# Performance work log

Measured on AMD Instinct MI355X. Metric: run time of the kernel, lower is better.

## Reference

```python
import jax, jax.numpy as jnp
import numpy as np
from jax import lax

B, C = 16, 80
LEVELS = [(100, 128), (50, 64), (25, 32), (13, 16), (7, 8)]
STRIDES = [8, 16, 32, 64, 128]
SCORE_THR = 0.05
IOU_THR = 0.6
MAX_DET = 1000


def make_coords(h, w, stride):
    # FCOS: center of each cell in original-image coordinates, order (x, y)
    ys = jnp.arange(h, dtype=jnp.float32) * stride + stride // 2
    xs = jnp.arange(w, dtype=jnp.float32) * stride + stride // 2
    yy, xx = jnp.meshgrid(ys, xs, indexing='ij')
    return jnp.stack([xx.reshape(-1), yy.reshape(-1)], axis=-1)  # [h*w, 2]


def flatten_levels(feats):
    # list of [B, c, h, w] -> [B, sum(h*w), c]
    return jnp.concatenate(
        [f.transpose(0, 2, 3, 1).reshape(f.shape[0], -1, f.shape[1]) for f in feats], axis=1)


def pairwise_iou(boxes):
    # boxes [N,4]; +1 area convention, matching the torch box_nms
    x1, y1, x2, y2 = boxes[:, 0], boxes[:, 1], boxes[:, 2], boxes[:, 3]
    areas = (x2 - x1 + 1.0) * (y2 - y1 + 1.0)
    xmin = jnp.maximum(x1[:, None], x1[None, :])
    ymin = jnp.maximum(y1[:, None], y1[None, :])
    xmax = jnp.minimum(x2[:, None], x2[None, :])
    ymax = jnp.minimum(y2[:, None], y2[None, :])
    inter = jnp.clip(xmax - xmin, 0.0) * jnp.clip(ymax - ymin, 0.0)
    return inter / (areas[:, None] + areas[None, :] - inter)


def nms_keep_mask(boxes, valid, thr):
    # boxes are sorted by descending score (top_k sorted=True) -> greedy order = index order
    n = boxes.shape[0]
    iou = pairwise_iou(boxes)
    idx = jnp.arange(n)

    def body(i, sup):
        kept = jnp.logical_not(sup[i])
        return sup | (kept & (iou[i] > thr) & (idx > i))

    sup = lax.fori_loop(0, n, body, jnp.logical_not(valid))
    return valid & jnp.logical_not(sup)


def detect_forward(cls_feats, ctr_feats, reg_feats):
    cls_logits = flatten_levels(cls_feats)   # [B, P, C]
    ctr_logits = flatten_levels(ctr_feats)   # [B, P, 1]
    reg_preds = flatten_levels(reg_feats)    # [B, P, 4] (l, t, r, b)
    coords = jnp.concatenate(
        [make_coords(h, w, s) for (h, w), s in zip(LEVELS, STRIDES)], axis=0)  # [P, 2]

    cls_preds = jax.nn.sigmoid(cls_logits)
    ctr_preds = jax.nn.sigmoid(ctr_logits)[..., 0]
    cls_scores = jnp.max(cls_preds, axis=-1) * ctr_preds        # add_centerness=True
    cls_classes = jnp.argmax(cls_preds, axis=-1) + 1            # [B, P] int

    boxes = jnp.concatenate(
        [coords[None] - reg_preds[..., :2], coords[None] + reg_preds[..., 2:]], axis=-1)

    max_num = min(MAX_DET, cls_scores.shape[-1])
    scores_topk, topk_ind = lax.top_k(cls_scores, max_num)      # sorted descending
    classes_topk = jnp.take_along_axis(cls_classes, topk_ind, axis=1)
    boxes_topk = jnp.take_along_axis(boxes, topk_ind[..., None], axis=1)

    valid = scores_topk >= SCORE_THR
    # batched_nms class-offset trick
    max_coord = jnp.max(boxes_topk, axis=(1, 2), keepdims=True)
    offs = classes_topk.astype(boxes_topk.dtype)[..., None] * (max_coord + 1.0)
    boxes_for_nms = boxes_topk + offs

    keep = jax.vmap(lambda b, v: nms_keep_mask(b, v, IOU_THR))(boxes_for_nms, valid)
    keep_f = keep.astype(scores_topk.dtype)
    # fixed-shape masked outputs (torch version returns ragged per-batch lists)
    return scores_topk * keep_f, classes_topk * keep, boxes_topk * keep_f[..., None]


def setup_inputs() -> dict:
    key = jax.random.key(0)
    ks = jax.random.split(key, 3 * len(LEVELS))
    inp = {}
    for i, (h, w) in enumerate(LEVELS):
        inp[f'cls{i}'] = jax.random.normal(ks[3 * i], (B, C, h, w), jnp.float32)
        inp[f'ctr{i}'] = jax.random.normal(ks[3 * i + 1], (B, 1, h, w), jnp.float32)
        # positive ltrb offsets of plausible magnitude
        inp[f'reg{i}'] = jax.random.uniform(ks[3 * i + 2], (B, 4, h, w), jnp.float32) * 64.0 + 1.0
    return inp


def reference(cls0, cls1, cls2, cls3, cls4, ctr0, ctr1, ctr2, ctr3, ctr4,
              reg0, reg1, reg2, reg3, reg4):
    return detect_forward([cls0, cls1, cls2, cls3, cls4],
                          [ctr0, ctr1, ctr2, ctr3, ctr4],
                          [reg0, reg1, reg2, reg3, reg4])
```

## Files before the change

### kernel.cpp

```cpp
#include <hip/hip_runtime.h>
#include <stdint.h>

#define NANCH 17064
#define BATCH 16
#define NCLS 80
#define KDET 1000
#define SCORE_THR 0.05f
#define IOU_THR 0.6f

typedef unsigned long long u64;
typedef unsigned int u32;

__device__ __forceinline__ float sigf(float x) { return 1.0f / (1.0f + expf(-x)); }

__device__ __forceinline__ void decode_anchor(int n, int& l, int& h, int& w) {
  if (n < 12800)      { l = 0; h = n >> 7;               w = n & 127; }
  else if (n < 16000) { l = 1; int r = n - 12800; h = r >> 6; w = r & 63; }
  else if (n < 16800) { l = 2; int r = n - 16000; h = r >> 5; w = r & 31; }
  else if (n < 17008) { l = 3; int r = n - 16800; h = r >> 4; w = r & 15; }
  else                { l = 4; int r = n - 17008; h = r >> 3; w = r & 7; }
}

__device__ __forceinline__ u32 fenc(float f) {
  u32 u = __float_as_uint(f);
  return (u & 0x80000000u) ? ~u : (u | 0x80000000u);
}
__device__ __forceinline__ float fdec(u32 e) {
  u32 u = (e & 0x80000000u) ? (e ^ 0x80000000u) : ~e;
  return __uint_as_float(u);
}

__global__ __launch_bounds__(256, 4) void k_score(
    const float* __restrict__ cls0, const float* __restrict__ ctr0,
    const float* __restrict__ cls1, const float* __restrict__ ctr1,
    const float* __restrict__ cls2, const float* __restrict__ ctr2,
    const float* __restrict__ cls3, const float* __restrict__ ctr3,
    const float* __restrict__ cls4, const float* __restrict__ ctr4,
    u32* __restrict__ sb, u32* __restrict__ cl8)
{
  __shared__ float sm[4][64][5];
  __shared__ u32 sa[4][64];

  const int x = threadIdx.x;
  const int y = threadIdx.y;
  const int b = blockIdx.y;
  int q = blockIdx.x * 64 + x;
  const bool act = (q < NANCH / 4);
  int qc = act ? q : (NANCH / 4 - 1);
  int n = qc * 4;

  const float* cp; const float* tp; int hw, off;
  if (n < 12800)      { cp = cls0; tp = ctr0; hw = 12800; off = n; }
  else if (n < 16000) { cp = cls1; tp = ctr1; hw = 3200;  off = n - 12800; }
  else if (n < 16800) { cp = cls2; tp = ctr2; hw = 800;   off = n - 16000; }
  else if (n < 17008) { cp = cls3; tp = ctr3; hw = 208;   off = n - 16800; }
  else                { cp = cls4; tp = ctr4; hw = 56;    off = n - 17008; }
  const float4* base = (const float4*)(cp + (size_t)b * NCLS * hw + off);
  const int s4 = hw >> 2;
  const int cb = y * 20;

  float4 v[20];
#pragma unroll
  for (int cc = 0; cc < 20; ++cc) v[cc] = base[(size_t)(cb + cc) * s4];

  float m0 = -1.0f, m1 = -1.0f, m2 = -1.0f, m3 = -1.0f;
  int a0 = 0, a1 = 0, a2 = 0, a3 = 0;
#pragma unroll
  for (int cc = 0; cc < 20; ++cc) {
    int c = cb + cc;
    float s;
    s = sigf(v[cc].x); if (s > m0) { m0 = s; a0 = c; }
    s = sigf(v[cc].y); if (s > m1) { m1 = s; a1 = c; }
    s = sigf(v[cc].z); if (s > m2) { m2 = s; a2 = c; }
    s = sigf(v[cc].w); if (s > m3) { m3 = s; a3 = c; }
  }
  sm[y][x][0] = m0; sm[y][x][1] = m1; sm[y][x][2] = m2; sm[y][x][3] = m3;
  sa[y][x] = (u32)a0 | ((u32)a1 << 8) | ((u32)a2 << 16) | ((u32)a3 << 24);
  __syncthreads();

  if (y == 0 && act) {
#pragma unroll
    for (int k = 1; k < 4; ++k) {
      u32 pk = sa[k][x];
      float t;
      t = sm[k][x][0]; if (t > m0) { m0 = t; a0 = (int)(pk & 0xffu); }
      t = sm[k][x][1]; if (t > m1) { m1 = t; a1 = (int)((pk >> 8) & 0xffu); }
      t = sm[k][x][2]; if (t > m2) { m2 = t; a2 = (int)((pk >> 16) & 0xffu); }
      t = sm[k][x][3]; if (t > m3) { m3 = t; a3 = (int)((pk >> 24) & 0xffu); }
    }
    float4 ctv = *(const float4*)(tp + (size_t)b * hw + off);
    uint4 sv;
    sv.x = __float_as_uint(m0 * sigf(ctv.x));
    sv.y = __float_as_uint(m1 * sigf(ctv.y));
    sv.z = __float_as_uint(m2 * sigf(ctv.z));
    sv.w = __float_as_uint(m3 * sigf(ctv.w));
    *(uint4*)(sb + b * NANCH + n) = sv;
    cl8[(b * NANCH + n) >> 2] = (u32)a0 | ((u32)a1 << 8) | ((u32)a2 << 16) | ((u32)a3 << 24);
  }
}

__global__ __launch_bounds__(1024) void k_topk(
    const u32* __restrict__ sb,
    u64* __restrict__ candG, int* __restrict__ cntG, u32* __restrict__ maxcG)
{
  __shared__ u32 hist[1024];
  __shared__ u32 wtot[16];
  __shared__ int s_T1, s_above, s_T2, s_cnt;

  const int tid = threadIdx.x;
  const int b = blockIdx.x;
  const int lane = tid & 63, wv = tid >> 6;
  const u32* sbb = sb + b * NANCH;

  u32 sc[17];
#pragma unroll
  for (int k = 0; k < 17; ++k) {
    int n = tid + (k << 10);
    sc[k] = (n < NANCH) ? sbb[n] : 0u;
  }

  hist[tid] = 0;
  __syncthreads();
#pragma unroll
  for (int k = 0; k < 17; ++k) {
    int n = tid + (k << 10);
    if (n < NANCH) atomicAdd(&hist[sc[k] >> 22], 1u);
  }
  __syncthreads();
  u32 h = hist[tid];
  u32 s = h;
  for (int d = 1; d < 64; d <<= 1) { u32 y = (u32)__shfl_down((int)s, d); if (lane + d < 64) s += y; }
  if (lane == 0) wtot[wv] = s;
  hist[tid] = 0;
  __syncthreads();
  {
    u32 add = 0;
    for (int w2 = wv + 1; w2 < 16; ++w2) add += wtot[w2];
    s += add;
  }
  if (s >= (u32)KDET && s - h < (u32)KDET) { s_T1 = tid; s_above = (int)(s - h); }
  __syncthreads();
  const int T1 = s_T1; const int above = s_above;

#pragma unroll
  for (int k = 0; k < 17; ++k) {
    int n = tid + (k << 10);
    u32 bits = sc[k];
    if (n < NANCH && (int)(bits >> 22) == T1) atomicAdd(&hist[(bits >> 12) & 1023u], 1u);
  }
  __syncthreads();
  h = hist[tid];
  s = h;
  for (int d = 1; d < 64; d <<= 1) { u32 y = (u32)__shfl_down((int)s, d); if (lane + d < 64) s += y; }
  if (lane == 0) wtot[wv] = s;
  __syncthreads();
  {
    u32 add = 0;
    for (int w2 = wv + 1; w2 < 16; ++w2) add += wtot[w2];
    s += add;
  }
  if (above + (int)s >= KDET && above + (int)(s - h) < KDET) s_T2 = tid;
  if (tid == 0) s_cnt = 0;
  __syncthreads();
  const int T2 = s_T2;

#pragma unroll
  for (int k = 0; k < 17; ++k) {
    int n = tid + (k << 10);
    u32 bits = sc[k];
    int c1 = (int)(bits >> 22);
    bool cand = (n < NANCH) &&
                ((c1 > T1) || (c1 == T1 && (int)((bits >> 12) & 1023u) >= T2));
    if (cand) {
      int pos = atomicAdd(&s_cnt, 1);
      if (pos < 2048) candG[b * 2048 + pos] = ((u64)bits << 32) | (u64)(u32)(~(u32)n);
    }
  }
  __syncthreads();
  if (tid == 0) {
    int C = s_cnt; if (C > 2048) C = 2048;
    cntG[b] = C;
    maxcG[b] = 0u;
  }
}

__global__ __launch_bounds__(256) void k_rank(
    const float* __restrict__ reg0, const float* __restrict__ reg1,
    const float* __restrict__ reg2, const float* __restrict__ reg3,
    const float* __restrict__ reg4,
    const unsigned char* __restrict__ cl8,
    const u64* __restrict__ candG, const int* __restrict__ cntG,
    float* __restrict__ scoreG, int* __restrict__ clsG, float4* __restrict__ boxG,
    u32* __restrict__ maxcG)
{
  __shared__ ulonglong2 keys2[1024];
  const int tid = threadIdx.x;
  const int c = blockIdx.x;
  const int b = blockIdx.y;
  const int lane = tid & 63;
  const int C = cntG[b];
  const u64* cand = candG + b * 2048;

  for (int i = tid; i < 1024; i += 256) {
    int i0 = 2 * i, i1 = 2 * i + 1;
    ulonglong2 v;
    v.x = (i0 < C) ? cand[i0] : 0ull;
    v.y = (i1 < C) ? cand[i1] : 0ull;
    keys2[i] = v;
  }
  __syncthreads();

  const int idx = c * 256 + tid;
  const bool active = (idx < C);
  u64 key = active ? cand[idx] : 0ull;

  int cnt = 0;
  const int Cp2 = ((C + 7) >> 3) << 2;
  for (int s = 0; s < Cp2; s += 4) {
    ulonglong2 a0 = keys2[s], a1 = keys2[s + 1], a2 = keys2[s + 2], a3 = keys2[s + 3];
    cnt += (a0.x > key) + (a0.y > key) + (a1.x > key) + (a1.y > key)
         + (a2.x > key) + (a2.y > key) + (a3.x > key) + (a3.y > key);
  }

  u32 enc = 0u;
  if (active && cnt < KDET) {
    u32 bits = (u32)(key >> 32);
    int n = (int)(~(u32)(key & 0xFFFFFFFFull));
    float score = __uint_as_float(bits);
    int clsv = (int)cl8[b * NANCH + n] + 1;
    int l, hh, ww; decode_anchor(n, l, hh, ww);
    const float* rp; int W, ST, HF, hw;
    switch (l) {
      case 0: rp = reg0; W = 128; ST = 8;   HF = 4;  hw = 12800; break;
      case 1: rp = reg1; W = 64;  ST = 16;  HF = 8;  hw = 3200;  break;
      case 2: rp = reg2; W = 32;  ST = 32;  HF = 16; hw = 800;   break;
      case 3: rp = reg3; W = 16;  ST = 64;  HF = 32; hw = 208;   break;
      default: rp = reg4; W = 8;  ST = 128; HF = 64; hw = 56;    break;
    }
    float cx = (float)(ww * ST + HF);
    float cy = (float)(hh * ST + HF);
    const float* rb = rp + (size_t)b * 4 * hw + hh * W + ww;
    float r0 = rb[0], r1 = rb[hw], r2 = rb[2 * hw], r3 = rb[3 * hw];
    float4 bx = make_float4(cx - r0, cy - r1, cx + r2, cy + r3);
    int o = b * KDET + cnt;
    scoreG[o] = score; clsG[o] = clsv; boxG[o] = bx;
    enc = fenc(fmaxf(fmaxf(bx.x, bx.y), fmaxf(bx.z, bx.w)));
  }
  for (int d = 32; d > 0; d >>= 1) {
    u32 o = (u32)__shfl_xor((int)enc, d);
    enc = (o > enc) ? o : enc;
  }
  if (lane == 0 && enc != 0u) atomicMax(maxcG + b, enc);
}

__global__ __launch_bounds__(256) void k_mat(
    const float4* __restrict__ boxG, const int* __restrict__ clsG,
    const u32* __restrict__ maxcG, u64* __restrict__ mat)
{
  const int tid = threadIdx.x, lane = tid & 63, wv = tid >> 6;
  const int b = blockIdx.y;
  const int tile = blockIdx.x * 4 + wv;
  if (tile >= 136) return;
  int rt = 0, rem = tile;
  while (rem >= rt + 1) { rem -= rt + 1; ++rt; }
  const int wc = rem;

  const float scale = fdec(maxcG[b]) + 1.0f;

  const int j = (wc << 6) + lane;
  float jx1 = 0, jy1 = 0, jx2 = 0, jy2 = 0, aj = 0;
  if (j < KDET) {
    float4 bj = boxG[b * KDET + j];
    float off = (float)clsG[b * KDET + j] * scale;
    jx1 = bj.x + off; jy1 = bj.y + off; jx2 = bj.z + off; jy2 = bj.w + off;
    aj = (jx2 - jx1 + 1.0f) * (jy2 - jy1 + 1.0f);
  }
  const int ri = (rt << 6) + lane;
  float ix1 = 0, iy1 = 0, ix2 = 0, iy2 = 0;
  if (ri < KDET) {
    float4 bi = boxG[b * KDET + ri];
    float off = (float)clsG[b * KDET + ri] * scale;
    ix1 = bi.x + off; iy1 = bi.y + off; ix2 = bi.z + off; iy2 = bi.w + off;
  }

  u64 myword = 0ull;
  for (int r = 0; r < 64; ++r) {
    float x1 = __shfl(ix1, r), y1 = __shfl(iy1, r);
    float x2 = __shfl(ix2, r), y2 = __shfl(iy2, r);
    float ai = (x2 - x1 + 1.0f) * (y2 - y1 + 1.0f);
    int row = (rt << 6) + r;
    float xmin = fmaxf(x1, jx1), ymin = fmaxf(y1, jy1);
    float xmax = fminf(x2, jx2), ymax = fminf(y2, jy2);
    float inter = fmaxf(xmax - xmin, 0.0f) * fmaxf(ymax - ymin, 0.0f);
    float iou = inter / ((ai + aj) - inter);
    bool p = (j < row) && (j < KDET) && (iou > IOU_THR);
    u64 mm = __ballot(p);
    if (lane == r) myword = mm;
  }
  const int rowl = (rt << 6) + lane;
  if (rowl < KDET) mat[(size_t)b * (KDET * 16) + rowl * 16 + wc] = myword;
}

__global__ __launch_bounds__(1024) void k_nms(
    const u64* __restrict__ mat, const float* __restrict__ scoreG,
    const int* __restrict__ clsG, const float4* __restrict__ boxG,
    float* __restrict__ out)
{
  __shared__ u64 keptS[16];
  __shared__ int s_chg;
  const int tid = threadIdx.x;
  const int b = blockIdx.x;
  const int wv = tid >> 6, lane = tid & 63;

  float sc = (tid < KDET) ? scoreG[b * KDET + tid] : 0.0f;
  bool valid = (tid < KDET) && (sc >= SCORE_THR);

  u64 row[16];
  const u64* mrow = mat + (size_t)b * (KDET * 16) + (size_t)tid * 16;
  const int wtop = tid >> 6;
#pragma unroll
  for (int w = 0; w < 16; ++w)
    row[w] = (tid < KDET && w <= wtop) ? mrow[w] : 0ull;

  {
    u64 mb = __ballot(valid);
    if (lane == 0) keptS[wv] = mb;
  }
  __syncthreads();

  for (int it = 0; it < KDET + 1; ++it) {
    u64 sup = 0;
#pragma unroll
    for (int w = 0; w < 16; ++w) sup |= keptS[w] & row[w];
    bool nk = valid && (sup == 0ull);
    u64 nw = __ballot(nk);
    if (tid == 0) s_chg = 0;
    __syncthreads();
    if (lane == 0) {
      if (nw != keptS[wv]) s_chg = 1;
      keptS[wv] = nw;
    }
    __syncthreads();
    if (s_chg == 0) break;
  }

  if (tid < KDET) {
    bool kp = ((keptS[tid >> 6] >> (tid & 63)) & 1ull) != 0ull;
    int o1 = b * KDET + tid;
    out[o1] = kp ? sc : 0.0f;
    out[BATCH * KDET + o1] = kp ? (float)clsG[o1] : 0.0f;
    float4 bx = boxG[o1];
    float* ob = out + 2 * BATCH * KDET + (size_t)o1 * 4;
    ob[0] = kp ? bx.x : 0.0f;
    ob[1] = kp ? bx.y : 0.0f;
    ob[2] = kp ? bx.z : 0.0f;
    ob[3] = kp ? bx.w : 0.0f;
  }
}

extern "C" void kernel_launch(void* const* d_in, const int* in_sizes, int n_in,
                              void* d_out, int out_size, void* d_ws, size_t ws_size,
                              hipStream_t stream) {
  const float* cls[5]; const float* ctr[5]; const float* reg[5];
  for (int i = 0; i < 5; ++i) {
    cls[i] = (const float*)d_in[3 * i + 0];
    ctr[i] = (const float*)d_in[3 * i + 1];
    reg[i] = (const float*)d_in[3 * i + 2];
  }
  char* ws = (char*)d_ws;
  u32* sb   = (u32*)ws;
  unsigned char* cl8 = (unsigned char*)(ws + 1092096);
  u64* candG = (u64*)(ws + 1365120);
  u64* mat  = (u64*)ws;
  float*  scoreG = (float*) (ws + 2048000);
  int*    clsG   = (int*)   (ws + 2112000);
  float4* boxG   = (float4*)(ws + 2176000);
  int*    cntG   = (int*)   (ws + 2432000);
  u32*    maxcG  = (u32*)   (ws + 2432064);

  dim3 g1((NANCH / 4 + 63) / 64, BATCH);
  k_score<<<g1, dim3(64, 4), 0, stream>>>(cls[0], ctr[0], cls[1], ctr[1], cls[2], ctr[2],
                                          cls[3], ctr[3], cls[4], ctr[4], sb, (u32*)cl8);
  k_topk<<<BATCH, 1024, 0, stream>>>(sb, candG, cntG, maxcG);
  k_rank<<<dim3(8, BATCH), 256, 0, stream>>>(reg[0], reg[1], reg[2], reg[3], reg[4],
                                             cl8, candG, cntG, scoreG, clsG, boxG, maxcG);
  k_mat<<<dim3(34, BATCH), 256, 0, stream>>>(boxG, clsG, maxcG, mat);
  k_nms<<<BATCH, 1024, 0, stream>>>(mat, scoreG, clsG, boxG, (float*)d_out);
}
```

Before: 197.6 us.

## Privatize top-k histograms, read rank keys from global, skip zero NMS words

The top-k kernel splits each histogram into 8 interleaved sub-histograms so fewer threads contend for the same LDS atomic, and sums the copies before the scan. The rank kernel no longer stages candidate keys in shared memory; every thread reads them straight from global memory (uniform addresses, served from cache) and loops only up to the exact count. The NMS fixed-point loop skips bitmask words above the thread's own wave, which are always zero. In exchange the top-k kernel uses 8x more LDS and an extra reduction, and the rank kernel relies on cache-served scalar or broadcast loads.

After: 218.8 us. +10.7%, slower.

```diff
diff --git a/kernel.cpp b/kernel.cpp
--- a/kernel.cpp
+++ b/kernel.cpp
@@ -103,13 +103,14 @@
     const u32* __restrict__ sb,
     u64* __restrict__ candG, int* __restrict__ cntG, u32* __restrict__ maxcG)
 {
-  __shared__ u32 hist[1024];
+  __shared__ u32 subhist[8192];
   __shared__ u32 wtot[16];
   __shared__ int s_T1, s_above, s_T2, s_cnt;
 
   const int tid = threadIdx.x;
   const int b = blockIdx.x;
   const int lane = tid & 63, wv = tid >> 6;
+  const int cpy = tid & 7;
   const u32* sbb = sb + b * NANCH;
 
   u32 sc[17];
@@ -119,19 +120,24 @@
     sc[k] = (n < NANCH) ? sbb[n] : 0u;
   }
 
-  hist[tid] = 0;
+#pragma unroll
+  for (int k = 0; k < 8; ++k) subhist[tid + (k << 10)] = 0;
   __syncthreads();
 #pragma unroll
   for (int k = 0; k < 17; ++k) {
     int n = tid + (k << 10);
-    if (n < NANCH) atomicAdd(&hist[sc[k] >> 22], 1u);
-  }
-  __syncthreads();
-  u32 h = hist[tid];
+    if (n < NANCH) atomicAdd(&subhist[((sc[k] >> 22) << 3) + cpy], 1u);
+  }
+  __syncthreads();
+  u32 h = 0;
+#pragma unroll
+  for (int c = 0; c < 8; ++c) h += subhist[(tid << 3) + c];
+  __syncthreads();
+#pragma unroll
+  for (int k = 0; k < 8; ++k) subhist[tid + (k << 10)] = 0;
   u32 s = h;
   for (int d = 1; d < 64; d <<= 1) { u32 y = (u32)__shfl_down((int)s, d); if (lane + d < 64) s += y; }
   if (lane == 0) wtot[wv] = s;
-  hist[tid] = 0;
   __syncthreads();
   {
     u32 add = 0;
@@ -146,10 +152,13 @@
   for (int k = 0; k < 17; ++k) {
     int n = tid + (k << 10);
     u32 bits = sc[k];
-    if (n < NANCH && (int)(bits >> 22) == T1) atomicAdd(&hist[(bits >> 12) & 1023u], 1u);
-  }
-  __syncthreads();
-  h = hist[tid];
+    if (n < NANCH && (int)(bits >> 22) == T1)
+      atomicAdd(&subhist[(((bits >> 12) & 1023u) << 3) + cpy], 1u);
+  }
+  __syncthreads();
+  h = 0;
+#pragma unroll
+  for (int c = 0; c < 8; ++c) h += subhist[(tid << 3) + c];
   s = h;
   for (int d = 1; d < 64; d <<= 1) { u32 y = (u32)__shfl_down((int)s, d); if (lane + d < 64) s += y; }
   if (lane == 0) wtot[wv] = s;
@@ -193,34 +202,26 @@
     float* __restrict__ scoreG, int* __restrict__ clsG, float4* __restrict__ boxG,
     u32* __restrict__ maxcG)
 {
-  __shared__ ulonglong2 keys2[1024];
   const int tid = threadIdx.x;
   const int c = blockIdx.x;
   const int b = blockIdx.y;
   const int lane = tid & 63;
   const int C = cntG[b];
-  const u64* cand = candG + b * 2048;
-
-  for (int i = tid; i < 1024; i += 256) {
-    int i0 = 2 * i, i1 = 2 * i + 1;
-    ulonglong2 v;
-    v.x = (i0 < C) ? cand[i0] : 0ull;
-    v.y = (i1 < C) ? cand[i1] : 0ull;
-    keys2[i] = v;
-  }
-  __syncthreads();
+  const u64* __restrict__ cand = candG + b * 2048;
 
   const int idx = c * 256 + tid;
   const bool active = (idx < C);
   u64 key = active ? cand[idx] : 0ull;
 
   int cnt = 0;
-  const int Cp2 = ((C + 7) >> 3) << 2;
-  for (int s = 0; s < Cp2; s += 4) {
-    ulonglong2 a0 = keys2[s], a1 = keys2[s + 1], a2 = keys2[s + 2], a3 = keys2[s + 3];
-    cnt += (a0.x > key) + (a0.y > key) + (a1.x > key) + (a1.y > key)
-         + (a2.x > key) + (a2.y > key) + (a3.x > key) + (a3.y > key);
-  }
+  int s = 0;
+  for (; s + 8 <= C; s += 8) {
+    u64 k0 = cand[s],     k1 = cand[s + 1], k2 = cand[s + 2], k3 = cand[s + 3];
+    u64 k4 = cand[s + 4], k5 = cand[s + 5], k6 = cand[s + 6], k7 = cand[s + 7];
+    cnt += (int)(k0 > key) + (int)(k1 > key) + (int)(k2 > key) + (int)(k3 > key)
+         + (int)(k4 > key) + (int)(k5 > key) + (int)(k6 > key) + (int)(k7 > key);
+  }
+  for (; s < C; ++s) cnt += (int)(cand[s] > key);
 
   u32 enc = 0u;
   if (active && cnt < KDET) {
@@ -331,7 +332,8 @@
   for (int it = 0; it < KDET + 1; ++it) {
     u64 sup = 0;
 #pragma unroll
-    for (int w = 0; w < 16; ++w) sup |= keptS[w] & row[w];
+    for (int w = 0; w < 16; ++w)
+      if (w <= wtop) sup |= keptS[w] & row[w];
     bool nk = valid && (sup == 0ull);
     u64 nw = __ballot(nk);
     if (tid == 0) s_chg = 0;
```
